# Performance work log

Measured on AMD Instinct MI355X. Metric: run time of the kernel, lower is better.

## Reference

```python
import jax, jax.numpy as jnp
import numpy as np

FP8_MAX = 448.0  # e4m3 max
SCALE_MARGIN = 0.8


def _fp8_quant_dequant(t, scale):
    # scaled value is <= 448*0.8 by construction, so no saturation/overflow
    q = (t / scale).astype(jnp.float8_e4m3fn)
    return q.astype(jnp.float32) * scale


def setup_inputs() -> dict:
    key = jax.random.key(0)
    k1, k2 = jax.random.split(key)
    B, S, D_IN, D_OUT = 4, 2048, 2048, 2048
    x = jax.random.normal(k1, (B, S, D_IN), dtype=jnp.float32)
    weight = jax.random.normal(k2, (D_OUT, D_IN), dtype=jnp.float32)
    bias = jnp.zeros((D_OUT,), dtype=jnp.float32)
    return {"x": x, "weight": weight, "bias": bias}


def reference(x, weight, bias):
    # Shared FP8ScalingManager: amax history = [amax_x] for x, then [amax_x, amax_w] for w.
    amax_x = jnp.max(jnp.abs(x))
    amax_w = jnp.max(jnp.abs(weight))
    x_scale = amax_x / (FP8_MAX * SCALE_MARGIN)
    w_scale = jnp.maximum(amax_x, amax_w) / (FP8_MAX * SCALE_MARGIN)  # history max
    x_scale = jax.lax.stop_gradient(x_scale)  # .item() detaches in torch
    w_scale = jax.lax.stop_gradient(w_scale)
    # quantize to fp8 e4m3, dequantize, scaled matmul (math of torch._scaled_mm)
    x_dq = _fp8_quant_dequant(x, x_scale)      # [B,S,Din]
    w_dq = _fp8_quant_dequant(weight, w_scale)  # [Dout,Din]
    out = jnp.einsum('bsd,od->bso', x_dq, w_dq)  # [B,S,Dout]
    return out + bias
```

## Files before the change

kernel.cpp:

```cpp
#include <hip/hip_runtime.h>
#include <stdint.h>

typedef float v4f __attribute__((ext_vector_type(4)));
typedef int v8i __attribute__((ext_vector_type(8)));

#define FP8_DENOM 358.4f


__device__ __forceinline__ unsigned pack4_fp8(float a, float b, float c, float d) {
  int v = 0;
  v = __builtin_amdgcn_cvt_pk_fp8_f32(a, b, v, false);
  v = __builtin_amdgcn_cvt_pk_fp8_f32(c, d, v, true);
  return (unsigned)v;
}

__device__ __forceinline__ void gload_lds16(const void* g, void* l) {
  __builtin_amdgcn_global_load_lds(
      (const __attribute__((address_space(1))) uint32_t*)(uintptr_t)g,
      (__attribute__((address_space(3))) uint32_t*)(uint32_t)(uintptr_t)l,
      16, 0, 0);
}


__global__ void __launch_bounds__(256) amax_part(const float4* __restrict__ x,
                                                 const float4* __restrict__ w,
                                                 float* __restrict__ part) {
  const int b = blockIdx.x, t = threadIdx.x;
  const float4* p = (b < 1024) ? x : w;
  const long base = (long)((b < 1024) ? b : (b - 1024)) * 4096;
  float m0 = 0.f, m1 = 0.f, m2 = 0.f, m3 = 0.f;
#pragma unroll
  for (int j = 0; j < 4; ++j) {
    float4 v0 = p[base + (j * 4 + 0) * 256 + t];
    float4 v1 = p[base + (j * 4 + 1) * 256 + t];
    float4 v2 = p[base + (j * 4 + 2) * 256 + t];
    float4 v3 = p[base + (j * 4 + 3) * 256 + t];
    m0 = fmaxf(m0, fmaxf(fmaxf(fabsf(v0.x), fabsf(v0.y)), fmaxf(fabsf(v0.z), fabsf(v0.w))));
    m1 = fmaxf(m1, fmaxf(fmaxf(fabsf(v1.x), fabsf(v1.y)), fmaxf(fabsf(v1.z), fabsf(v1.w))));
    m2 = fmaxf(m2, fmaxf(fmaxf(fabsf(v2.x), fabsf(v2.y)), fmaxf(fabsf(v2.z), fabsf(v2.w))));
    m3 = fmaxf(m3, fmaxf(fmaxf(fabsf(v3.x), fabsf(v3.y)), fmaxf(fabsf(v3.z), fabsf(v3.w))));
  }
  float m = fmaxf(fmaxf(m0, m1), fmaxf(m2, m3));
#pragma unroll
  for (int off = 32; off > 0; off >>= 1)
    m = fmaxf(m, __shfl_down(m, off, 64));
  __shared__ float red[4];
  const int lane = t & 63, wvid = t >> 6;
  if (lane == 0) red[wvid] = m;
  __syncthreads();
  if (t == 0) part[b] = fmaxf(fmaxf(red[0], red[1]), fmaxf(red[2], red[3]));
}


__global__ void __launch_bounds__(256) scale_reduce(const float* __restrict__ part,
                                                    unsigned* __restrict__ amax) {
  const int t = threadIdx.x;
  float mx = fmaxf(fmaxf(part[t], part[t + 256]), fmaxf(part[t + 512], part[t + 768]));
  float mw = part[1024 + t];
#pragma unroll
  for (int off = 32; off > 0; off >>= 1) {
    mx = fmaxf(mx, __shfl_down(mx, off, 64));
    mw = fmaxf(mw, __shfl_down(mw, off, 64));
  }
  __shared__ float rx[4], rw[4];
  const int lane = t & 63, wvid = t >> 6;
  if (lane == 0) { rx[wvid] = mx; rw[wvid] = mw; }
  __syncthreads();
  if (t == 0) {
    const float ax = fmaxf(fmaxf(rx[0], rx[1]), fmaxf(rx[2], rx[3]));
    const float aw = fmaxf(fmaxf(rw[0], rw[1]), fmaxf(rw[2], rw[3]));
    const float sx = ax / FP8_DENOM;
    const float sw = fmaxf(ax, aw) / FP8_DENOM;
    amax[0] = __float_as_uint(ax);
    amax[1] = __float_as_uint(aw);
    amax[2] = __float_as_uint(1.0f / sx);
    amax[3] = __float_as_uint(1.0f / sw);
    amax[4] = __float_as_uint(sx * sw);
  }
}


__global__ void quant2_kernel(const float4* __restrict__ x, uint4* __restrict__ xq, int nx16,
                              const float4* __restrict__ w, uint4* __restrict__ wq, int nw16,
                              int xblocks, const unsigned* __restrict__ amax) {
  const int isw = ((int)blockIdx.x >= xblocks) ? 1 : 0;
  const float rs = __uint_as_float(amax[2 + isw]);
  const float4* in = isw ? w : x;
  uint4* outq = isw ? wq : xq;
  const int n16 = isw ? nw16 : nx16;
  const int b0 = isw ? ((int)blockIdx.x - xblocks) : (int)blockIdx.x;
  const int nb = isw ? ((int)gridDim.x - xblocks) : xblocks;
  const long stride = (long)nb * blockDim.x;
  for (long i = (long)b0 * blockDim.x + threadIdx.x; i < n16; i += stride) {
    float4 v0 = in[4 * i + 0], v1 = in[4 * i + 1], v2 = in[4 * i + 2], v3 = in[4 * i + 3];
    uint4 r;
    r.x = pack4_fp8(v0.x * rs, v0.y * rs, v0.z * rs, v0.w * rs);
    r.y = pack4_fp8(v1.x * rs, v1.y * rs, v1.z * rs, v1.w * rs);
    r.z = pack4_fp8(v2.x * rs, v2.y * rs, v2.z * rs, v2.w * rs);
    r.w = pack4_fp8(v3.x * rs, v3.y * rs, v3.z * rs, v3.w * rs);
    outq[i] = r;
  }
}


__global__ void __launch_bounds__(256) gemm_mx(
    const uint8_t* __restrict__ Aq, const uint8_t* __restrict__ Bq,
    const float* __restrict__ bias, float* __restrict__ out,
    const unsigned* __restrict__ amax) {
  constexpr int K = 2048, N = 2048, BK = 128, ITERS = K / BK;
  __shared__ alignas(16) uint8_t sA[2][128 * BK];
  __shared__ alignas(16) uint8_t sB[2][128 * BK];

  const int tid = threadIdx.x;
  const int lane = tid & 63;
  const int wid = tid >> 6;
  const int wy = wid >> 1, wx = wid & 1;
  const long tileM = (long)blockIdx.y * 128;
  const long tileN = (long)blockIdx.x * 128;

  v4f acc[4][4];
#pragma unroll
  for (int i = 0; i < 4; ++i)
#pragma unroll
    for (int j = 0; j < 4; ++j) acc[i][j] = (v4f)(0.f);

  const int srow = tid >> 3;
  const int schunk = (tid & 7) ^ (srow & 7);
  const uint8_t* gA = Aq + (tileM + srow) * K + schunk * 16;
  const uint8_t* gB = Bq + (tileN + srow) * K + schunk * 16;

  const int q = lane >> 4;
  const int mrow = lane & 15;

  int aoff[4][2], boff[4][2];
#pragma unroll
  for (int i = 0; i < 4; ++i) {
    const int rA = wy * 64 + i * 16 + mrow, swA = rA & 7;
    aoff[i][0] = rA * 128 + 16 * ((2 * q) ^ swA);
    aoff[i][1] = rA * 128 + 16 * ((2 * q + 1) ^ swA);
    const int rB = wx * 64 + i * 16 + mrow, swB = rB & 7;
    boff[i][0] = rB * 128 + 16 * ((2 * q) ^ swB);
    boff[i][1] = rB * 128 + 16 * ((2 * q + 1) ^ swB);
  }

  auto stage = [&](int buf, int k0) {
#pragma unroll
    for (int s = 0; s < 4; ++s) {
      gload_lds16(gA + (long)s * 32 * K + k0, &sA[buf][s * 4096 + tid * 16]);
      gload_lds16(gB + (long)s * 32 * K + k0, &sB[buf][s * 4096 + tid * 16]);
    }
  };

  stage(0, 0);
  for (int it = 0; it < ITERS; ++it) {
    __syncthreads();
    if (it + 1 < ITERS) stage((it + 1) & 1, (it + 1) * BK);

    const uint8_t* bufA = sA[it & 1];
    const uint8_t* bufB = sB[it & 1];
    union Frag { v8i v; uint4 h[2]; };
    Frag a[4], b[4];
#pragma unroll
    for (int i = 0; i < 4; ++i) {
      a[i].h[0] = *(const uint4*)(bufA + aoff[i][0]);
      a[i].h[1] = *(const uint4*)(bufA + aoff[i][1]);
      b[i].h[0] = *(const uint4*)(bufB + boff[i][0]);
      b[i].h[1] = *(const uint4*)(bufB + boff[i][1]);
    }
#pragma unroll
    for (int i = 0; i < 4; ++i)
#pragma unroll
      for (int j = 0; j < 4; ++j)
        acc[i][j] = __builtin_amdgcn_mfma_scale_f32_16x16x128_f8f6f4(
            a[i].v, b[j].v, acc[i][j],  0,  0,
             0, 0x7F7F7F7F,  0, 0x7F7F7F7F);
  }

  const float scale = __uint_as_float(amax[4]);
#pragma unroll
  for (int j = 0; j < 4; ++j) {
    const long col = tileN + wx * 64 + j * 16 + mrow;
    const float bv = bias[col];
#pragma unroll
    for (int i = 0; i < 4; ++i) {
      const long row = tileM + wy * 64 + i * 16 + q * 4;
#pragma unroll
      for (int r = 0; r < 4; ++r)
        out[(row + r) * N + col] = acc[i][j][r] * scale + bv;
    }
  }
}


extern "C" void kernel_launch(void* const* d_in, const int* in_sizes, int n_in,
                              void* d_out, int out_size, void* d_ws, size_t ws_size,
                              hipStream_t stream) {
  const float* x = (const float*)d_in[0];
  const float* w = (const float*)d_in[1];
  const float* bias = (const float*)d_in[2];
  float* out = (float*)d_out;

  const int M = 8192, N = 2048, K = 2048;
  const long nx = (long)M * K, nw = (long)N * K;

  unsigned* amax = (unsigned*)d_ws;
  float* part = (float*)((uint8_t*)d_ws + 256);
  uint8_t* xq = (uint8_t*)d_ws + 8192;
  uint8_t* wq = xq + nx;

  amax_part<<<1280, 256, 0, stream>>>((const float4*)x, (const float4*)w, part);
  scale_reduce<<<1, 256, 0, stream>>>(part, amax);
  quant2_kernel<<<5120, 256, 0, stream>>>((const float4*)x, (uint4*)xq, (int)(nx / 16),
                                          (const float4*)w, (uint4*)wq, (int)(nw / 16),
                                          4096, amax);
  gemm_mx<<<dim3(N / 128, M / 128), 256, 0, stream>>>(xq, wq, bias, out, amax);
}
```

Before: 175.3 us.

## Enlarge GEMM tile to 256x256, fuse amax reduction via atomics, simplify quantize

```diff
diff --git a/kernel.cpp b/kernel.cpp
--- a/kernel.cpp
+++ b/kernel.cpp
@@ -24,7 +24,7 @@
 
 __global__ void __launch_bounds__(256) amax_part(const float4* __restrict__ x,
                                                  const float4* __restrict__ w,
-                                                 float* __restrict__ part) {
+                                                 unsigned* __restrict__ amax) {
   const int b = blockIdx.x, t = threadIdx.x;
   const float4* p = (b < 1024) ? x : w;
   const long base = (long)((b < 1024) ? b : (b - 1024)) * 4096;
@@ -48,79 +48,51 @@
   const int lane = t & 63, wvid = t >> 6;
   if (lane == 0) red[wvid] = m;
   __syncthreads();
-  if (t == 0) part[b] = fmaxf(fmaxf(red[0], red[1]), fmaxf(red[2], red[3]));
+  if (t == 0)
+    atomicMax(amax + ((b < 1024) ? 0 : 1),
+              __float_as_uint(fmaxf(fmaxf(red[0], red[1]), fmaxf(red[2], red[3]))));
 }
 
 
-__global__ void __launch_bounds__(256) scale_reduce(const float* __restrict__ part,
-                                                    unsigned* __restrict__ amax) {
+__global__ void __launch_bounds__(256) quant2_kernel(
+    const float4* __restrict__ x, unsigned* __restrict__ xq,
+    const float4* __restrict__ w, unsigned* __restrict__ wq,
+    const unsigned* __restrict__ amax) {
   const int t = threadIdx.x;
-  float mx = fmaxf(fmaxf(part[t], part[t + 256]), fmaxf(part[t + 512], part[t + 768]));
-  float mw = part[1024 + t];
+  const int isw = ((int)blockIdx.x >= 4096) ? 1 : 0;
+  const float ax = __uint_as_float(amax[0]);
+  const float aw = __uint_as_float(amax[1]);
+  const float s = (isw ? fmaxf(ax, aw) : ax) / FP8_DENOM;
+  const float rs = 1.0f / s;
+  const float4* in = isw ? w : x;
+  unsigned* outq = isw ? wq : xq;
+  const long base = (long)(isw ? ((int)blockIdx.x - 4096) : (int)blockIdx.x) * 1024;
 #pragma unroll
-  for (int off = 32; off > 0; off >>= 1) {
-    mx = fmaxf(mx, __shfl_down(mx, off, 64));
-    mw = fmaxf(mw, __shfl_down(mw, off, 64));
-  }
-  __shared__ float rx[4], rw[4];
-  const int lane = t & 63, wvid = t >> 6;
-  if (lane == 0) { rx[wvid] = mx; rw[wvid] = mw; }
-  __syncthreads();
-  if (t == 0) {
-    const float ax = fmaxf(fmaxf(rx[0], rx[1]), fmaxf(rx[2], rx[3]));
-    const float aw = fmaxf(fmaxf(rw[0], rw[1]), fmaxf(rw[2], rw[3]));
-    const float sx = ax / FP8_DENOM;
-    const float sw = fmaxf(ax, aw) / FP8_DENOM;
-    amax[0] = __float_as_uint(ax);
-    amax[1] = __float_as_uint(aw);
-    amax[2] = __float_as_uint(1.0f / sx);
-    amax[3] = __float_as_uint(1.0f / sw);
-    amax[4] = __float_as_uint(sx * sw);
+  for (int j = 0; j < 4; ++j) {
+    float4 v = in[base + j * 256 + t];
+    outq[base + j * 256 + t] = pack4_fp8(v.x * rs, v.y * rs, v.z * rs, v.w * rs);
   }
 }
 
 
-__global__ void quant2_kernel(const float4* __restrict__ x, uint4* __restrict__ xq, int nx16,
-                              const float4* __restrict__ w, uint4* __restrict__ wq, int nw16,
-                              int xblocks, const unsigned* __restrict__ amax) {
-  const int isw = ((int)blockIdx.x >= xblocks) ? 1 : 0;
-  const float rs = __uint_as_float(amax[2 + isw]);
-  const float4* in = isw ? w : x;
-  uint4* outq = isw ? wq : xq;
-  const int n16 = isw ? nw16 : nx16;
-  const int b0 = isw ? ((int)blockIdx.x - xblocks) : (int)blockIdx.x;
-  const int nb = isw ? ((int)gridDim.x - xblocks) : xblocks;
-  const long stride = (long)nb * blockDim.x;
-  for (long i = (long)b0 * blockDim.x + threadIdx.x; i < n16; i += stride) {
-    float4 v0 = in[4 * i + 0], v1 = in[4 * i + 1], v2 = in[4 * i + 2], v3 = in[4 * i + 3];
-    uint4 r;
-    r.x = pack4_fp8(v0.x * rs, v0.y * rs, v0.z * rs, v0.w * rs);
-    r.y = pack4_fp8(v1.x * rs, v1.y * rs, v1.z * rs, v1.w * rs);
-    r.z = pack4_fp8(v2.x * rs, v2.y * rs, v2.z * rs, v2.w * rs);
-    r.w = pack4_fp8(v3.x * rs, v3.y * rs, v3.z * rs, v3.w * rs);
-    outq[i] = r;
-  }
-}
-
-
-__global__ void __launch_bounds__(256) gemm_mx(
+__global__ void __launch_bounds__(512, 2) gemm_mx(
     const uint8_t* __restrict__ Aq, const uint8_t* __restrict__ Bq,
     const float* __restrict__ bias, float* __restrict__ out,
     const unsigned* __restrict__ amax) {
   constexpr int K = 2048, N = 2048, BK = 128, ITERS = K / BK;
-  __shared__ alignas(16) uint8_t sA[2][128 * BK];
-  __shared__ alignas(16) uint8_t sB[2][128 * BK];
+  __shared__ alignas(16) uint8_t sA[2][256 * BK];
+  __shared__ alignas(16) uint8_t sB[2][256 * BK];
 
   const int tid = threadIdx.x;
   const int lane = tid & 63;
   const int wid = tid >> 6;
-  const int wy = wid >> 1, wx = wid & 1;
-  const long tileM = (long)blockIdx.y * 128;
-  const long tileN = (long)blockIdx.x * 128;
+  const int wy = wid >> 2, wx = wid & 3;
+  const long tileM = (long)blockIdx.y * 256;
+  const long tileN = (long)blockIdx.x * 256;
 
-  v4f acc[4][4];
+  v4f acc[8][4];
 #pragma unroll
-  for (int i = 0; i < 4; ++i)
+  for (int i = 0; i < 8; ++i)
 #pragma unroll
     for (int j = 0; j < 4; ++j) acc[i][j] = (v4f)(0.f);
 
@@ -131,23 +103,17 @@
 
   const int q = lane >> 4;
   const int mrow = lane & 15;
-
-  int aoff[4][2], boff[4][2];
-#pragma unroll
-  for (int i = 0; i < 4; ++i) {
-    const int rA = wy * 64 + i * 16 + mrow, swA = rA & 7;
-    aoff[i][0] = rA * 128 + 16 * ((2 * q) ^ swA);
-    aoff[i][1] = rA * 128 + 16 * ((2 * q + 1) ^ swA);
-    const int rB = wx * 64 + i * 16 + mrow, swB = rB & 7;
-    boff[i][0] = rB * 128 + 16 * ((2 * q) ^ swB);
-    boff[i][1] = rB * 128 + 16 * ((2 * q + 1) ^ swB);
-  }
+  const int sw = mrow & 7;
+  const int aoff0 = (wy * 128 + mrow) * BK + 16 * ((2 * q) ^ sw);
+  const int aoff1 = (wy * 128 + mrow) * BK + 16 * ((2 * q + 1) ^ sw);
+  const int boff0 = (wx * 64 + mrow) * BK + 16 * ((2 * q) ^ sw);
+  const int boff1 = (wx * 64 + mrow) * BK + 16 * ((2 * q + 1) ^ sw);
 
   auto stage = [&](int buf, int k0) {
 #pragma unroll
     for (int s = 0; s < 4; ++s) {
-      gload_lds16(gA + (long)s * 32 * K + k0, &sA[buf][s * 4096 + tid * 16]);
-      gload_lds16(gB + (long)s * 32 * K + k0, &sB[buf][s * 4096 + tid * 16]);
+      gload_lds16(gA + (long)s * 64 * K + k0, &sA[buf][s * 8192 + tid * 16]);
+      gload_lds16(gB + (long)s * 64 * K + k0, &sB[buf][s * 8192 + tid * 16]);
     }
   };
 
@@ -159,31 +125,37 @@
     const uint8_t* bufA = sA[it & 1];
     const uint8_t* bufB = sB[it & 1];
     union Frag { v8i v; uint4 h[2]; };
-    Frag a[4], b[4];
+    Frag b[4];
 #pragma unroll
-    for (int i = 0; i < 4; ++i) {
-      a[i].h[0] = *(const uint4*)(bufA + aoff[i][0]);
-      a[i].h[1] = *(const uint4*)(bufA + aoff[i][1]);
-      b[i].h[0] = *(const uint4*)(bufB + boff[i][0]);
-      b[i].h[1] = *(const uint4*)(bufB + boff[i][1]);
+    for (int j = 0; j < 4; ++j) {
+      b[j].h[0] = *(const uint4*)(bufB + boff0 + j * 16 * BK);
+      b[j].h[1] = *(const uint4*)(bufB + boff1 + j * 16 * BK);
     }
+    __builtin_amdgcn_s_setprio(1);
 #pragma unroll
-    for (int i = 0; i < 4; ++i)
+    for (int i = 0; i < 8; ++i) {
+      Frag a;
+      a.h[0] = *(const uint4*)(bufA + aoff0 + i * 16 * BK);
+      a.h[1] = *(const uint4*)(bufA + aoff1 + i * 16 * BK);
 #pragma unroll
       for (int j = 0; j < 4; ++j)
         acc[i][j] = __builtin_amdgcn_mfma_scale_f32_16x16x128_f8f6f4(
-            a[i].v, b[j].v, acc[i][j],  0,  0,
+            a.v, b[j].v, acc[i][j],  0,  0,
              0, 0x7F7F7F7F,  0, 0x7F7F7F7F);
+    }
+    __builtin_amdgcn_s_setprio(0);
   }
 
-  const float scale = __uint_as_float(amax[4]);
+  const float ax = __uint_as_float(amax[0]);
+  const float aw = __uint_as_float(amax[1]);
+  const float scale = (ax / FP8_DENOM) * (fmaxf(ax, aw) / FP8_DENOM);
 #pragma unroll
   for (int j = 0; j < 4; ++j) {
     const long col = tileN + wx * 64 + j * 16 + mrow;
     const float bv = bias[col];
 #pragma unroll
-    for (int i = 0; i < 4; ++i) {
-      const long row = tileM + wy * 64 + i * 16 + q * 4;
+    for (int i = 0; i < 8; ++i) {
+      const long row = tileM + wy * 128 + i * 16 + q * 4;
 #pragma unroll
       for (int r = 0; r < 4; ++r)
         out[(row + r) * N + col] = acc[i][j][r] * scale + bv;
@@ -201,17 +173,15 @@
   float* out = (float*)d_out;
 
   const int M = 8192, N = 2048, K = 2048;
-  const long nx = (long)M * K, nw = (long)N * K;
+  const long nx = (long)M * K;
 
   unsigned* amax = (unsigned*)d_ws;
-  float* part = (float*)((uint8_t*)d_ws + 256);
   uint8_t* xq = (uint8_t*)d_ws + 8192;
   uint8_t* wq = xq + nx;
 
-  amax_part<<<1280, 256, 0, stream>>>((const float4*)x, (const float4*)w, part);
-  scale_reduce<<<1, 256, 0, stream>>>(part, amax);
-  quant2_kernel<<<5120, 256, 0, stream>>>((const float4*)x, (uint4*)xq, (int)(nx / 16),
-                                          (const float4*)w, (uint4*)wq, (int)(nw / 16),
-                                          4096, amax);
-  gemm_mx<<<dim3(N / 128, M / 128), 256, 0, stream>>>(xq, wq, bias, out, amax);
+  hipMemsetAsync(amax, 0, 8, stream);
+  amax_part<<<1280, 256, 0, stream>>>((const float4*)x, (const float4*)w, amax);
+  quant2_kernel<<<5120, 256, 0, stream>>>((const float4*)x, (unsigned*)xq,
+                                          (const float4*)w, (unsigned*)wq, amax);
+  gemm_mx<<<dim3(N / 256, M / 256), 512, 0, stream>>>(xq, wq, bias, out, amax);
 }
```

After: 177.7 us. Within noise of the previous version (+1.4%).
